# Performance work log

Hardware: AMD Instinct MI355X
Metric: run time of the kernel (lower is better)

## Reference

```python
import jax, jax.numpy as jnp
import numpy as np

B, T, H, OUT = 16384, 128, 256, 10
EPS = 1e-5


def setup_inputs() -> dict:
    key = jax.random.key(0)
    ks = jax.random.split(key, 8)
    x = jax.random.randint(ks[0], (B, T, 1), 0, 10).astype(jnp.float32)
    def lin(k, fan_out, fan_in):
        bound = 1.0 / np.sqrt(fan_in)
        kw, kb = jax.random.split(k)
        w = jax.random.uniform(kw, (fan_out, fan_in), jnp.float32, -bound, bound)
        b = jax.random.uniform(kb, (fan_out,), jnp.float32, -bound, bound)
        return w, b
    embed_w, embed_b = lin(ks[1], H, 1)
    update_w, update_b = lin(ks[2], H, H)
    out_w, out_b = lin(ks[3], OUT, H)
    return {
        "x": x,
        "embed_w": embed_w, "embed_b": embed_b,
        "update_w": update_w, "update_b": update_b,
        "gamma": jnp.ones((H,), jnp.float32), "beta": jnp.zeros((H,), jnp.float32),
        "out_w": out_w, "out_b": out_b,
    }


def _layer_norm(h, gamma, beta):
    mu = jnp.mean(h, axis=-1, keepdims=True)
    var = jnp.mean(jnp.square(h - mu), axis=-1, keepdims=True)
    return (h - mu) * jax.lax.rsqrt(var + EPS) * gamma + beta


def reference(x, embed_w, embed_b, update_w, update_b, gamma, beta, out_w, out_b):
    # embed is per-timestep independent -> precompute for all T at once: [B,T,H]
    inp_all = jnp.tanh(jnp.einsum('bti,hi->bth', x, embed_w) + embed_b)

    def step(h, inp_t):  # h:[B,H], inp_t:[B,H]
        h = jnp.tanh((inp_t + h) @ update_w.T + update_b)
        h = _layer_norm(h, gamma, beta)
        return h, None

    h0 = jnp.zeros((x.shape[0], embed_w.shape[0]), x.dtype)
    h, _ = jax.lax.scan(step, h0, jnp.swapaxes(inp_all, 0, 1))  # scan over T
    return h @ out_w.T + out_b  # [B, 10]
```

## Files before the change

kernel.cpp:

```cpp
#include <hip/hip_runtime.h>
#include <hip/hip_fp16.h>
#include <math.h>

typedef _Float16 f16;
typedef _Float16 f16x2 __attribute__((ext_vector_type(2)));
typedef _Float16 f16x8 __attribute__((ext_vector_type(8)));
typedef float f32x4 __attribute__((ext_vector_type(4)));
typedef unsigned char u8;

#define HDIM 256
#define TST 128
#define OUTD 10
#define S2LE 2.8853900817779268f

static __device__ __forceinline__ f16x2 pkrtz(float a, float b) {
  auto r = __builtin_amdgcn_cvt_pkrtz(a, b);
  return *(f16x2*)&r;
}

__global__ __launch_bounds__(256, 2) void rnn_kernel(
    const float* __restrict__ x,
    const float* __restrict__ embed_w,
    const float* __restrict__ embed_b,
    const float* __restrict__ update_w,
    const float* __restrict__ update_b,
    const float* __restrict__ gamma,
    const float* __restrict__ beta,
    const float* __restrict__ out_w,
    const float* __restrict__ out_b,
    float* __restrict__ out)
{
  __shared__ __align__(16) f16   sFR[2][8][64][8];
  __shared__ __align__(16) float sD1[10 * 260];
  __shared__ __align__(16) float sBW[HDIM];
  __shared__ __align__(16) float sRSg[HDIM];
  __shared__ float sOB[16];
  __shared__ u8    sXb[TST][32];

  const int tid = threadIdx.x;
  const int w  = tid >> 6;
  const int l  = tid & 63;
  const int q  = l >> 4;
  const int ml = l & 15;
  const int base = blockIdx.x * 32;
  const int nb = w * 64 + q * 4;
  const int m3 = ml & 3;
  const int srcl = ((ml >> 2) << 4) + ml;

  float* T0 = (float*)&sFR[0][0][0][0];

  {
    float ew = embed_w[tid], eb = embed_b[tid];
    #pragma unroll
    for (int xv = 0; xv < 10; xv++)
      T0[tid * 10 + xv] = tanhf((float)xv * ew + eb);
  }
  for (int idx = tid; idx < 32 * TST; idx += 256) {
    int col = idx >> 7, tt = idx & 127;
    sXb[tt][col] = (u8)(int)x[(size_t)(base + col) * TST + tt];
  }
  if (tid < 16) {
    float v = 0.f;
    if (tid < OUTD) {
      v = out_b[tid];
      const float* orow = out_w + tid * HDIM;
      for (int k = 0; k < HDIM; k += 4) {
        float4 wv = *(const float4*)(orow + k);
        float4 bv = *(const float4*)(beta + k);
        v = fmaf(wv.x, bv.x, fmaf(wv.y, bv.y, fmaf(wv.z, bv.z, fmaf(wv.w, bv.w, v))));
      }
    }
    sOB[tid] = v;
  }
  __syncthreads();

  {
    const int n = tid;
    const float* wrow = update_w + n * HDIM;
    float ty[10];
    #pragma unroll
    for (int xv = 0; xv < 10; xv++) ty[xv] = 0.f;
    float bw = 0.f, rsg = 0.f;
    for (int k = 0; k < HDIM; k += 4) {
      float4 wv4 = *(const float4*)(wrow + k);
      float4 b4  = *(const float4*)(beta + k);
      float4 g4  = *(const float4*)(gamma + k);
      bw  = fmaf(wv4.x, b4.x, fmaf(wv4.y, b4.y, fmaf(wv4.z, b4.z, fmaf(wv4.w, b4.w, bw))));
      rsg = fmaf(wv4.x, S2LE * g4.x, fmaf(wv4.y, S2LE * g4.y,
            fmaf(wv4.z, S2LE * g4.z, fmaf(wv4.w, S2LE * g4.w, rsg))));
      #pragma unroll
      for (int kk = 0; kk < 4; kk++) {
        float wv = ((const float*)&wv4)[kk];
        const float* t0r = T0 + (k + kk) * 10;
        #pragma unroll
        for (int xv = 0; xv < 10; xv++) ty[xv] = fmaf(wv, t0r[xv], ty[xv]);
      }
    }
    float ubn = update_b[n];
    sBW[n]  = S2LE * bw;
    sRSg[n] = rsg;
    #pragma unroll
    for (int xv = 0; xv < 10; xv++)
      sD1[xv * 260 + n] = S2LE * (ty[xv] + ubn + bw);
  }
  __syncthreads();

  f16x8 wf[4][8];
  #pragma unroll
  for (int c = 0; c < 8; c++) {
    const int k0 = c * 32 + q * 4;
    float4 g0 = *(const float4*)(gamma + k0);
    float4 g1 = *(const float4*)(gamma + k0 + 16);
    #pragma unroll
    for (int nt = 0; nt < 4; nt++) {
      const float* wrow = update_w + (w * 64 + nt * 16 + ml) * HDIM;
      float4 a0 = *(const float4*)(wrow + k0);
      float4 a1 = *(const float4*)(wrow + k0 + 16);
      f16x8 f;
      f[0]=(f16)(S2LE*g0.x*a0.x); f[1]=(f16)(S2LE*g0.y*a0.y);
      f[2]=(f16)(S2LE*g0.z*a0.z); f[3]=(f16)(S2LE*g0.w*a0.w);
      f[4]=(f16)(S2LE*g1.x*a1.x); f[5]=(f16)(S2LE*g1.y*a1.y);
      f[6]=(f16)(S2LE*g1.z*a1.z); f[7]=(f16)(S2LE*g1.w*a1.w);
      wf[nt][c] = f;
    }
  }
  f32x4 rsgr[4];
  #pragma unroll
  for (int nt = 0; nt < 4; nt++)
    rsgr[nt] = *(const f32x4*)(sRSg + nb + nt * 16);

  f16x8 ones_;
  #pragma unroll
  for (int j = 0; j < 8; j++) ones_[j] = (f16)1.f;

  f32x4 acc0[4], acc1[4];
  float s1A = 0.f, s2A = 0.f, s1B = 0.f, s2B = 0.f;

  {
    #pragma unroll
    for (int g = 0; g < 2; g++) {
      const int xv0 = (int)sXb[0][g * 16 + ml];
      const float* dp = sD1 + xv0 * 260;
      #pragma unroll
      for (int cp = 0; cp < 2; cp++) {
        union { f16x8 v8; f16x2 v2[4]; } pk;
        #pragma unroll
        for (int h = 0; h < 2; h++) {
          const int nt = 2 * cp + h;
          f32x4 dd = *(const f32x4*)(dp + nb + nt * 16);
          f32x4 bw = *(const f32x4*)(sBW + nb + nt * 16);
          float tq[4];
          #pragma unroll
          for (int r = 0; r < 4; r++) {
            float y = dd[r] - bw[r];
            float e = __builtin_amdgcn_exp2f(y);
            float tv = fmaf(-2.f, __builtin_amdgcn_rcpf(e + 1.f), 1.f);
            tq[r] = tv;
          }
          pk.v2[2 * h]     = pkrtz(tq[0], tq[1]);
          pk.v2[2 * h + 1] = pkrtz(tq[2], tq[3]);
        }
        *(f16x8*)&sFR[g][2 * w + cp][l][0] = pk.v8;
      }
    }
    __syncthreads();
  }

#define MMG3(FB, CC, CUR, NXT, ACC, AG, AS)                                    \
    { if ((CC) < 7) NXT = *(const f16x8*)((FB) + ((CC) + 1) * 512 + l * 8);    \
      ACC[0] = __builtin_amdgcn_mfma_f32_16x16x32_f16(wf[0][CC], CUR, ACC[0],0,0,0); \
      ACC[1] = __builtin_amdgcn_mfma_f32_16x16x32_f16(wf[1][CC], CUR, ACC[1],0,0,0); \
      ACC[2] = __builtin_amdgcn_mfma_f32_16x16x32_f16(wf[2][CC], CUR, ACC[2],0,0,0); \
      ACC[3] = __builtin_amdgcn_mfma_f32_16x16x32_f16(wf[3][CC], CUR, ACC[3],0,0,0); \
      AG = __builtin_amdgcn_mfma_f32_16x16x32_f16(CUR, CUR, AG, 0, 0, 0);      \
      AS = __builtin_amdgcn_mfma_f32_16x16x32_f16(ones_, CUR, AS, 0, 0, 0); }

#define SLICE(S, ACCE)                                                         \
    { _Pragma("unroll") for (int r_ = 0; r_ < 4; r_++) {                       \
        float y_ = fmaf(rs_, ACCE[S][r_], fmaf(-rm_, rsgr[S][r_], dd_[S][r_]));\
        float e_ = __builtin_amdgcn_exp2f(y_);                                 \
        tv_[S][r_] = fmaf(-2.f, __builtin_amdgcn_rcpf(e_ + 1.f), 1.f); } }

#define PACK(GE, CP)                                                           \
    { union { f16x8 v8; f16x2 v2[4]; } k_;                                     \
      k_.v2[0] = pkrtz(tv_[2*(CP)][0],   tv_[2*(CP)][1]);                      \
      k_.v2[1] = pkrtz(tv_[2*(CP)][2],   tv_[2*(CP)][3]);                      \
      k_.v2[2] = pkrtz(tv_[2*(CP)+1][0], tv_[2*(CP)+1][1]);                    \
      k_.v2[3] = pkrtz(tv_[2*(CP)+1][2], tv_[2*(CP)+1][3]);                    \
      *(f16x8*)&sFR[GE][2 * w + (CP)][l][0] = k_.v8; }

#define PHASE(TE, GM, GE, XOFF, ACCM, ACCE, S1E, S2E, S1O, S2O)                \
  {                                                                            \
    const int xv_ = (int)sXb[TE][XOFF + ml];                                   \
    const float* dp_ = sD1 + xv_ * 260 + nb;                                   \
    f32x4 dd_[4];                                                              \
    _Pragma("unroll") for (int n_ = 0; n_ < 4; n_++)                           \
      dd_[n_] = *(const f32x4*)(dp_ + n_ * 16);                                \
    const f16* fbm_ = &sFR[GM][0][0][0];                                       \
    f16x8 rA_ = *(const f16x8*)(fbm_ + l * 8);                                 \
    f16x8 rB_;                                                                 \
    f32x4 aG_ = {0.f,0.f,0.f,0.f}, aS_ = {0.f,0.f,0.f,0.f};                    \
    _Pragma("unroll") for (int n_ = 0; n_ < 4; n_++)                           \
      ACCM[n_] = (f32x4){0.f, 0.f, 0.f, 0.f};                                  \
    f32x4 tv_[4];                                                              \
    __builtin_amdgcn_s_setprio(1);                                             \
    MMG3(fbm_, 0, rA_, rB_, ACCM, aG_, aS_)                                    \
    MMG3(fbm_, 1, rB_, rA_, ACCM, aG_, aS_)                                    \
    float mu_ = (S1E) * (1.f / 256.f);                                         \
    float rs_ = __frsqrt_rn(fmaf((S2E), 1.f / 256.f, -mu_ * mu_) + 1e-5f);     \
    float rm_ = rs_ * mu_;                                                     \
    SLICE(0, ACCE)                                                             \
    MMG3(fbm_, 2, rA_, rB_, ACCM, aG_, aS_)                                    \
    MMG3(fbm_, 3, rB_, rA_, ACCM, aG_, aS_)                                    \
    SLICE(1, ACCE)                                                             \
    PACK(GE, 0)                                                                \
    MMG3(fbm_, 4, rA_, rB_, ACCM, aG_, aS_)                                    \
    MMG3(fbm_, 5, rB_, rA_, ACCM, aG_, aS_)                                    \
    SLICE(2, ACCE)                                                             \
    MMG3(fbm_, 6, rA_, rB_, ACCM, aG_, aS_)                                    \
    MMG3(fbm_, 7, rB_, rA_, ACCM, aG_, aS_)                                    \
    SLICE(3, ACCE)                                                             \
    PACK(GE, 1)                                                                \
    __builtin_amdgcn_s_setprio(0);                                             \
    __syncthreads();                                                           \
    S1O = aS_[0];                                                              \
    float sel_ = aG_[0];                                                       \
    sel_ = (m3 == 1) ? aG_[1] : sel_;                                          \
    sel_ = (m3 == 2) ? aG_[2] : sel_;                                          \
    sel_ = (m3 == 3) ? aG_[3] : sel_;                                          \
    S2O = __shfl(sel_, srcl, 64);                                              \
  }

  {
    const f16* fbm_ = &sFR[0][0][0][0];
    f16x8 rA_ = *(const f16x8*)(fbm_ + l * 8);
    f16x8 rB_;
    f32x4 aG_ = {0.f,0.f,0.f,0.f}, aS_ = {0.f,0.f,0.f,0.f};
    #pragma unroll
    for (int n_ = 0; n_ < 4; n_++) acc0[n_] = (f32x4){0.f, 0.f, 0.f, 0.f};
    MMG3(fbm_, 0, rA_, rB_, acc0, aG_, aS_)
    MMG3(fbm_, 1, rB_, rA_, acc0, aG_, aS_)
    MMG3(fbm_, 2, rA_, rB_, acc0, aG_, aS_)
    MMG3(fbm_, 3, rB_, rA_, acc0, aG_, aS_)
    MMG3(fbm_, 4, rA_, rB_, acc0, aG_, aS_)
    MMG3(fbm_, 5, rB_, rA_, acc0, aG_, aS_)
    MMG3(fbm_, 6, rA_, rB_, acc0, aG_, aS_)
    MMG3(fbm_, 7, rB_, rA_, acc0, aG_, aS_)
    __syncthreads();
    s1A = aS_[0];
    float sel_ = aG_[0];
    sel_ = (m3 == 1) ? aG_[1] : sel_;
    sel_ = (m3 == 2) ? aG_[2] : sel_;
    sel_ = (m3 == 3) ? aG_[3] : sel_;
    s2A = __shfl(sel_, srcl, 64);
  }

  #pragma unroll 1
  for (int t = 1; t <= 127; t++) {
    PHASE(t, 1, 0, 0,  acc1, acc0, s1A, s2A, s1B, s2B)
    PHASE(t, 0, 1, 16, acc0, acc1, s1B, s2B, s1A, s2A)
  }

  {
    f32x4 aG2 = {0.f,0.f,0.f,0.f}, aS2 = {0.f,0.f,0.f,0.f};
    const f16* fb1 = &sFR[1][0][0][0];
    #pragma unroll
    for (int c = 0; c < 8; c++) {
      f16x8 rr = *(const f16x8*)(fb1 + c * 512 + l * 8);
      aG2 = __builtin_amdgcn_mfma_f32_16x16x32_f16(rr, rr, aG2, 0, 0, 0);
      aS2 = __builtin_amdgcn_mfma_f32_16x16x32_f16(ones_, rr, aS2, 0, 0, 0);
    }
    float s1C = aS2[0];
    float sel2 = aG2[0];
    sel2 = (m3 == 1) ? aG2[1] : sel2;
    sel2 = (m3 == 2) ? aG2[2] : sel2;
    sel2 = (m3 == 3) ? aG2[3] : sel2;
    float s2C = __shfl(sel2, srcl, 64);

    float rsF[2], nmF[2];
    {
      float mu = s1A * (1.f / 256.f);
      float ve = fmaf(s2A, 1.f / 256.f, -mu * mu) + 1e-5f;
      rsF[0] = __frsqrt_rn(ve); nmF[0] = -rsF[0] * mu;
      float mu1 = s1C * (1.f / 256.f);
      float ve1 = fmaf(s2C, 1.f / 256.f, -mu1 * mu1) + 1e-5f;
      rsF[1] = __frsqrt_rn(ve1); nmF[1] = -rsF[1] * mu1;
    }
    f16x8 fin[2][2];
    #pragma unroll
    for (int g = 0; g < 2; g++)
      #pragma unroll
      for (int cp = 0; cp < 2; cp++)
        fin[g][cp] = *(const f16x8*)&sFR[g][2 * w + cp][l][0];

    f16* sOW = (f16*)sD1;
    for (int idx = tid; idx < 512; idx += 256) {
      int c = idx >> 6, l2 = idx & 63, q2 = l2 >> 4, o = l2 & 15;
      int k0 = c * 32 + q2 * 4;
      f16x8 f;
      #pragma unroll
      for (int j = 0; j < 8; j++) f[j] = (f16)0.f;
      if (o < OUTD) {
        const float* orow = out_w + o * HDIM;
        float4 a0 = *(const float4*)(orow + k0);
        float4 a1 = *(const float4*)(orow + k0 + 16);
        float4 g0 = *(const float4*)(gamma + k0);
        float4 g1 = *(const float4*)(gamma + k0 + 16);
        f[0]=(f16)(g0.x*a0.x); f[1]=(f16)(g0.y*a0.y); f[2]=(f16)(g0.z*a0.z); f[3]=(f16)(g0.w*a0.w);
        f[4]=(f16)(g1.x*a1.x); f[5]=(f16)(g1.y*a1.y); f[6]=(f16)(g1.z*a1.z); f[7]=(f16)(g1.w*a1.w);
      }
      *(f16x8*)(sOW + idx * 8) = f;
    }
    __syncthreads();

    float* sOut = (float*)&sFR[0][0][0][0];
    #pragma unroll
    for (int g = 0; g < 2; g++) {
      f32x4 aO = {0.f, 0.f, 0.f, 0.f};
      #pragma unroll
      for (int cp = 0; cp < 2; cp++) {
        f16x8 af;
        #pragma unroll
        for (int j = 0; j < 8; j++)
          af[j] = (f16)fmaf(rsF[g], (float)fin[g][cp][j], nmF[g]);
        f16x8 of = *(const f16x8*)(sOW + ((size_t)(2 * w + cp) * 64 + l) * 8);
        aO = __builtin_amdgcn_mfma_f32_16x16x32_f16(of, af, aO, 0, 0, 0);
      }
      #pragma unroll
      for (int r = 0; r < 4; r++)
        sOut[((g * 4 + w) * 16 + ml) * 16 + q * 4 + r] = aO[r];
    }
    __syncthreads();
    for (int idx = tid; idx < 32 * OUTD; idx += 256) {
      int m = idx / OUTD, o = idx - m * OUTD;
      int g = m >> 4, mm = m & 15;
      float s = 0.f;
      #pragma unroll
      for (int ww = 0; ww < 4; ww++) s += sOut[((g * 4 + ww) * 16 + mm) * 16 + o];
      out[(size_t)(base + m) * OUTD + o] = s + sOB[o];
    }
  }
}

extern "C" void kernel_launch(void* const* d_in, const int* in_sizes, int n_in,
                              void* d_out, int out_size, void* d_ws, size_t ws_size,
                              hipStream_t stream) {
  const float* x   = (const float*)d_in[0];
  const float* ew  = (const float*)d_in[1];
  const float* eb  = (const float*)d_in[2];
  const float* uw  = (const float*)d_in[3];
  const float* ub  = (const float*)d_in[4];
  const float* g   = (const float*)d_in[5];
  const float* be  = (const float*)d_in[6];
  const float* ow  = (const float*)d_in[7];
  const float* ob  = (const float*)d_in[8];
  float* out = (float*)d_out;

  const int B = in_sizes[0] / TST;
  const int grid = B / 32;
  hipLaunchKernelGGL(rnn_kernel, dim3(grid), dim3(256), 0, stream,
                     x, ew, eb, uw, ub, g, be, ow, ob, out);
}
```

Before: 353.9 us.

## Split hidden dimension across eight waves with LDS-reduced layernorm statistics

Doubles the block to 512 threads (8 waves), so each wave owns 32 hidden units instead of 64. This halves the per-wave update-weight fragments held in registers and the MFMA work on each step's critical path. Because each wave now sees only a slice of the hidden state, the layernorm sum and sum-of-squares are computed per slice with MFMAs, written to a shared-memory table, and summed by every thread on the next phase. The intent is more waves per CU to hide latency and shorter per-step chains, at the cost of extra LDS traffic, more threads joining each per-step barrier, and a higher register-pressure target from launch_bounds(512,4).

```diff
diff --git a/kernel.cpp b/kernel.cpp
--- a/kernel.cpp
+++ b/kernel.cpp
@@ -18,7 +18,7 @@
   return *(f16x2*)&r;
 }
 
-__global__ __launch_bounds__(256, 2) void rnn_kernel(
+__global__ __launch_bounds__(512, 4) void rnn_kernel(
     const float* __restrict__ x,
     const float* __restrict__ embed_w,
     const float* __restrict__ embed_b,
@@ -34,6 +34,7 @@
   __shared__ __align__(16) float sD1[10 * 260];
   __shared__ __align__(16) float sBW[HDIM];
   __shared__ __align__(16) float sRSg[HDIM];
+  __shared__ __align__(16) float sST[2][16][10][2];
   __shared__ float sOB[16];
   __shared__ u8    sXb[TST][32];
 
@@ -42,20 +43,20 @@
   const int l  = tid & 63;
   const int q  = l >> 4;
   const int ml = l & 15;
+  const int m3 = ml & 3;
   const int base = blockIdx.x * 32;
-  const int nb = w * 64 + q * 4;
-  const int m3 = ml & 3;
-  const int srcl = ((ml >> 2) << 4) + ml;
+  const int nb = w * 32 + q * 4;
+  const int diagw = (q == (ml >> 2));
 
   float* T0 = (float*)&sFR[0][0][0][0];
 
-  {
+  if (tid < 256) {
     float ew = embed_w[tid], eb = embed_b[tid];
     #pragma unroll
     for (int xv = 0; xv < 10; xv++)
       T0[tid * 10 + xv] = tanhf((float)xv * ew + eb);
   }
-  for (int idx = tid; idx < 32 * TST; idx += 256) {
+  for (int idx = tid; idx < 32 * TST; idx += 512) {
     int col = idx >> 7, tt = idx & 127;
     sXb[tt][col] = (u8)(int)x[(size_t)(base + col) * TST + tt];
   }
@@ -74,7 +75,7 @@
   }
   __syncthreads();
 
-  {
+  if (tid < 256) {
     const int n = tid;
     const float* wrow = update_w + n * HDIM;
     float ty[10];
@@ -105,15 +106,15 @@
   }
   __syncthreads();
 
-  f16x8 wf[4][8];
+  f16x8 wf[2][8];
   #pragma unroll
   for (int c = 0; c < 8; c++) {
     const int k0 = c * 32 + q * 4;
     float4 g0 = *(const float4*)(gamma + k0);
     float4 g1 = *(const float4*)(gamma + k0 + 16);
     #pragma unroll
-    for (int nt = 0; nt < 4; nt++) {
-      const float* wrow = update_w + (w * 64 + nt * 16 + ml) * HDIM;
+    for (int nt = 0; nt < 2; nt++) {
+      const float* wrow = update_w + (w * 32 + nt * 16 + ml) * HDIM;
       float4 a0 = *(const float4*)(wrow + k0);
       float4 a1 = *(const float4*)(wrow + k0 + 16);
       f16x8 f;
@@ -124,178 +125,171 @@
       wf[nt][c] = f;
     }
   }
-  f32x4 rsgr[4];
-  #pragma unroll
-  for (int nt = 0; nt < 4; nt++)
-    rsgr[nt] = *(const f32x4*)(sRSg + nb + nt * 16);
-
-  f16x8 ones_;
-  #pragma unroll
-  for (int j = 0; j < 8; j++) ones_[j] = (f16)1.f;
-
-  f32x4 acc0[4], acc1[4];
-  float s1A = 0.f, s2A = 0.f, s1B = 0.f, s2B = 0.f;
+  f32x4 rsgr[2];
+  rsgr[0] = *(const f32x4*)(sRSg + nb);
+  rsgr[1] = *(const f32x4*)(sRSg + nb + 16);
+
+  f32x4 acc0[2], acc1[2];
 
   {
     #pragma unroll
     for (int g = 0; g < 2; g++) {
       const int xv0 = (int)sXb[0][g * 16 + ml];
       const float* dp = sD1 + xv0 * 260;
-      #pragma unroll
-      for (int cp = 0; cp < 2; cp++) {
-        union { f16x8 v8; f16x2 v2[4]; } pk;
-        #pragma unroll
-        for (int h = 0; h < 2; h++) {
-          const int nt = 2 * cp + h;
-          f32x4 dd = *(const f32x4*)(dp + nb + nt * 16);
-          f32x4 bw = *(const f32x4*)(sBW + nb + nt * 16);
-          float tq[4];
-          #pragma unroll
-          for (int r = 0; r < 4; r++) {
-            float y = dd[r] - bw[r];
-            float e = __builtin_amdgcn_exp2f(y);
-            float tv = fmaf(-2.f, __builtin_amdgcn_rcpf(e + 1.f), 1.f);
-            tq[r] = tv;
-          }
-          pk.v2[2 * h]     = pkrtz(tq[0], tq[1]);
-          pk.v2[2 * h + 1] = pkrtz(tq[2], tq[3]);
-        }
-        *(f16x8*)&sFR[g][2 * w + cp][l][0] = pk.v8;
+      f32x4 bw0 = *(const f32x4*)(sBW + nb);
+      f32x4 bw1 = *(const f32x4*)(sBW + nb + 16);
+      f32x4 dd0 = *(const f32x4*)(dp + nb);
+      f32x4 dd1 = *(const f32x4*)(dp + nb + 16);
+      float t0v[4], t1v[4];
+      #pragma unroll
+      for (int r = 0; r < 4; r++) {
+        float y0 = dd0[r] - bw0[r];
+        float e0 = __builtin_amdgcn_exp2f(y0);
+        t0v[r] = fmaf(-2.f, __builtin_amdgcn_rcpf(e0 + 1.f), 1.f);
+        float y1 = dd1[r] - bw1[r];
+        float e1 = __builtin_amdgcn_exp2f(y1);
+        t1v[r] = fmaf(-2.f, __builtin_amdgcn_rcpf(e1 + 1.f), 1.f);
       }
-    }
-    __syncthreads();
-  }
-
-#define MMG3(FB, CC, CUR, NXT, ACC, AG, AS)                                    \
+      union { f16x8 v8; f16x2 v2[4]; } pk;
+      pk.v2[0] = pkrtz(t0v[0], t0v[1]);
+      pk.v2[1] = pkrtz(t0v[2], t0v[3]);
+      pk.v2[2] = pkrtz(t1v[0], t1v[1]);
+      pk.v2[3] = pkrtz(t1v[2], t1v[3]);
+      *(f16x8*)&sFR[g][w][l][0] = pk.v8;
+    }
+    __syncthreads();
+  }
+
+#define MMG2(FB, CC, CUR, NXT, ACC)                                            \
     { if ((CC) < 7) NXT = *(const f16x8*)((FB) + ((CC) + 1) * 512 + l * 8);    \
       ACC[0] = __builtin_amdgcn_mfma_f32_16x16x32_f16(wf[0][CC], CUR, ACC[0],0,0,0); \
-      ACC[1] = __builtin_amdgcn_mfma_f32_16x16x32_f16(wf[1][CC], CUR, ACC[1],0,0,0); \
-      ACC[2] = __builtin_amdgcn_mfma_f32_16x16x32_f16(wf[2][CC], CUR, ACC[2],0,0,0); \
-      ACC[3] = __builtin_amdgcn_mfma_f32_16x16x32_f16(wf[3][CC], CUR, ACC[3],0,0,0); \
-      AG = __builtin_amdgcn_mfma_f32_16x16x32_f16(CUR, CUR, AG, 0, 0, 0);      \
-      AS = __builtin_amdgcn_mfma_f32_16x16x32_f16(ones_, CUR, AS, 0, 0, 0); }
-
-#define SLICE(S, ACCE)                                                         \
+      ACC[1] = __builtin_amdgcn_mfma_f32_16x16x32_f16(wf[1][CC], CUR, ACC[1],0,0,0); }
+
+#define STATMM(RO, AG, AS)                                                     \
+    { f16x8 ones_;                                                             \
+      _Pragma("unroll") for (int j_ = 0; j_ < 8; j_++) ones_[j_] = (f16)1.f;   \
+      AG = __builtin_amdgcn_mfma_f32_16x16x32_f16(RO, RO, AG, 0, 0, 0);        \
+      AS = __builtin_amdgcn_mfma_f32_16x16x32_f16(ones_, RO, AS, 0, 0, 0); }
+
+#define STATWR(G, AG, AS)                                                      \
+    { float sel_ = AG[0];                                                      \
+      sel_ = (m3 == 1) ? AG[1] : sel_;                                         \
+      sel_ = (m3 == 2) ? AG[2] : sel_;                                         \
+      sel_ = (m3 == 3) ? AG[3] : sel_;                                         \
+      if (diagw) *(float2*)&sST[G][ml][w][0] = make_float2(AS[0], sel_); }
+
+#define STATRD(G, S1, S2)                                                      \
+    { const float* sp_ = &sST[G][ml][0][0];                                    \
+      f32x4 a0_ = *(const f32x4*)(sp_);                                        \
+      f32x4 a1_ = *(const f32x4*)(sp_ + 4);                                    \
+      f32x4 a2_ = *(const f32x4*)(sp_ + 8);                                    \
+      f32x4 a3_ = *(const f32x4*)(sp_ + 12);                                   \
+      S1 = ((a0_[0] + a0_[2]) + (a1_[0] + a1_[2]))                             \
+         + ((a2_[0] + a2_[2]) + (a3_[0] + a3_[2]));                            \
+      S2 = ((a0_[1] + a0_[3]) + (a1_[1] + a1_[3]))                             \
+         + ((a2_[1] + a2_[3]) + (a3_[1] + a3_[3])); }
+
+#define SLICEH(H, ACCE, DD, TVV)                                               \
     { _Pragma("unroll") for (int r_ = 0; r_ < 4; r_++) {                       \
-        float y_ = fmaf(rs_, ACCE[S][r_], fmaf(-rm_, rsgr[S][r_], dd_[S][r_]));\
+        float y_ = fmaf(rs_, ACCE[H][r_], fmaf(-rm_, rsgr[H][r_], DD[r_]));    \
         float e_ = __builtin_amdgcn_exp2f(y_);                                 \
-        tv_[S][r_] = fmaf(-2.f, __builtin_amdgcn_rcpf(e_ + 1.f), 1.f); } }
-
-#define PACK(GE, CP)                                                           \
-    { union { f16x8 v8; f16x2 v2[4]; } k_;                                     \
-      k_.v2[0] = pkrtz(tv_[2*(CP)][0],   tv_[2*(CP)][1]);                      \
-      k_.v2[1] = pkrtz(tv_[2*(CP)][2],   tv_[2*(CP)][3]);                      \
-      k_.v2[2] = pkrtz(tv_[2*(CP)+1][0], tv_[2*(CP)+1][1]);                    \
-      k_.v2[3] = pkrtz(tv_[2*(CP)+1][2], tv_[2*(CP)+1][3]);                    \
-      *(f16x8*)&sFR[GE][2 * w + (CP)][l][0] = k_.v8; }
-
-#define PHASE(TE, GM, GE, XOFF, ACCM, ACCE, S1E, S2E, S1O, S2O)                \
+        TVV[r_] = fmaf(-2.f, __builtin_amdgcn_rcpf(e_ + 1.f), 1.f); } }
+
+#define PHASE(TE, GM, GE, XOFF, ACCM, ACCE)                                    \
   {                                                                            \
+    float s1_, s2_;                                                            \
+    STATRD(GE, s1_, s2_)                                                       \
     const int xv_ = (int)sXb[TE][XOFF + ml];                                   \
     const float* dp_ = sD1 + xv_ * 260 + nb;                                   \
-    f32x4 dd_[4];                                                              \
-    _Pragma("unroll") for (int n_ = 0; n_ < 4; n_++)                           \
-      dd_[n_] = *(const f32x4*)(dp_ + n_ * 16);                                \
+    f32x4 dd0_ = *(const f32x4*)(dp_);                                         \
+    f32x4 dd1_ = *(const f32x4*)(dp_ + 16);                                    \
     const f16* fbm_ = &sFR[GM][0][0][0];                                       \
+    f16x8 rOwn_ = *(const f16x8*)(fbm_ + w * 512 + l * 8);                     \
+    f32x4 aG_ = {0.f,0.f,0.f,0.f}, aS_ = {0.f,0.f,0.f,0.f};                    \
+    STATMM(rOwn_, aG_, aS_)                                                    \
     f16x8 rA_ = *(const f16x8*)(fbm_ + l * 8);                                 \
     f16x8 rB_;                                                                 \
-    f32x4 aG_ = {0.f,0.f,0.f,0.f}, aS_ = {0.f,0.f,0.f,0.f};                    \
-    _Pragma("unroll") for (int n_ = 0; n_ < 4; n_++)                           \
-      ACCM[n_] = (f32x4){0.f, 0.f, 0.f, 0.f};                                  \
-    f32x4 tv_[4];                                                              \
+    ACCM[0] = (f32x4){0.f, 0.f, 0.f, 0.f};                                     \
+    ACCM[1] = (f32x4){0.f, 0.f, 0.f, 0.f};                                     \
     __builtin_amdgcn_s_setprio(1);                                             \
-    MMG3(fbm_, 0, rA_, rB_, ACCM, aG_, aS_)                                    \
-    MMG3(fbm_, 1, rB_, rA_, ACCM, aG_, aS_)                                    \
-    float mu_ = (S1E) * (1.f / 256.f);                                         \
-    float rs_ = __frsqrt_rn(fmaf((S2E), 1.f / 256.f, -mu_ * mu_) + 1e-5f);     \
+    MMG2(fbm_, 0, rA_, rB_, ACCM)                                              \
+    MMG2(fbm_, 1, rB_, rA_, ACCM)                                              \
+    float mu_ = s1_ * (1.f / 256.f);                                           \
+    float rs_ = __frsqrt_rn(fmaf(s2_, 1.f / 256.f, -mu_ * mu_) + 1e-5f);       \
     float rm_ = rs_ * mu_;                                                     \
-    SLICE(0, ACCE)                                                             \
-    MMG3(fbm_, 2, rA_, rB_, ACCM, aG_, aS_)                                    \
-    MMG3(fbm_, 3, rB_, rA_, ACCM, aG_, aS_)                                    \
-    SLICE(1, ACCE)                                                             \
-    PACK(GE, 0)                                                                \
-    MMG3(fbm_, 4, rA_, rB_, ACCM, aG_, aS_)                                    \
-    MMG3(fbm_, 5, rB_, rA_, ACCM, aG_, aS_)                                    \
-    SLICE(2, ACCE)                                                             \
-    MMG3(fbm_, 6, rA_, rB_, ACCM, aG_, aS_)                                    \
-    MMG3(fbm_, 7, rB_, rA_, ACCM, aG_, aS_)                                    \
-    SLICE(3, ACCE)                                                             \
-    PACK(GE, 1)                                                                \
+    float t0_[4], t1_[4];                                                      \
+    MMG2(fbm_, 2, rA_, rB_, ACCM)                                              \
+    SLICEH(0, ACCE, dd0_, t0_)                                                 \
+    MMG2(fbm_, 3, rB_, rA_, ACCM)                                              \
+    MMG2(fbm_, 4, rA_, rB_, ACCM)                                              \
+    SLICEH(1, ACCE, dd1_, t1_)                                                 \
+    MMG2(fbm_, 5, rB_, rA_, ACCM)                                              \
+    {                                                                          \
+      union { f16x8 v8; f16x2 v2[4]; } k_;                                     \
+      k_.v2[0] = pkrtz(t0_[0], t0_[1]);                                        \
+      k_.v2[1] = pkrtz(t0_[2], t0_[3]);                                        \
+      k_.v2[2] = pkrtz(t1_[0], t1_[1]);                                        \
+      k_.v2[3] = pkrtz(t1_[2], t1_[3]);                                        \
+      *(f16x8*)&sFR[GE][w][l][0] = k_.v8;                                      \
+    }                                                                          \
+    MMG2(fbm_, 6, rA_, rB_, ACCM)                                              \
+    MMG2(fbm_, 7, rB_, rA_, ACCM)                                              \
     __builtin_amdgcn_s_setprio(0);                                             \
+    STATWR(GM, aG_, aS_)                                                       \
     __syncthreads();                                                           \
-    S1O = aS_[0];                                                              \
-    float sel_ = aG_[0];                                                       \
-    sel_ = (m3 == 1) ? aG_[1] : sel_;                                          \
-    sel_ = (m3 == 2) ? aG_[2] : sel_;                                          \
-    sel_ = (m3 == 3) ? aG_[3] : sel_;                                          \
-    S2O = __shfl(sel_, srcl, 64);                                              \
   }
 
   {
     const f16* fbm_ = &sFR[0][0][0][0];
+    f16x8 rOwn_ = *(const f16x8*)(fbm_ + w * 512 + l * 8);
+    f32x4 aG_ = {0.f,0.f,0.f,0.f}, aS_ = {0.f,0.f,0.f,0.f};
+    STATMM(rOwn_, aG_, aS_)
     f16x8 rA_ = *(const f16x8*)(fbm_ + l * 8);
     f16x8 rB_;
-    f32x4 aG_ = {0.f,0.f,0.f,0.f}, aS_ = {0.f,0.f,0.f,0.f};
-    #pragma unroll
-    for (int n_ = 0; n_ < 4; n_++) acc0[n_] = (f32x4){0.f, 0.f, 0.f, 0.f};
-    MMG3(fbm_, 0, rA_, rB_, acc0, aG_, aS_)
-    MMG3(fbm_, 1, rB_, rA_, acc0, aG_, aS_)
-    MMG3(fbm_, 2, rA_, rB_, acc0, aG_, aS_)
-    MMG3(fbm_, 3, rB_, rA_, acc0, aG_, aS_)
-    MMG3(fbm_, 4, rA_, rB_, acc0, aG_, aS_)
-    MMG3(fbm_, 5, rB_, rA_, acc0, aG_, aS_)
-    MMG3(fbm_, 6, rA_, rB_, acc0, aG_, aS_)
-    MMG3(fbm_, 7, rB_, rA_, acc0, aG_, aS_)
-    __syncthreads();
-    s1A = aS_[0];
-    float sel_ = aG_[0];
-    sel_ = (m3 == 1) ? aG_[1] : sel_;
-    sel_ = (m3 == 2) ? aG_[2] : sel_;
-    sel_ = (m3 == 3) ? aG_[3] : sel_;
-    s2A = __shfl(sel_, srcl, 64);
+    acc0[0] = (f32x4){0.f, 0.f, 0.f, 0.f};
+    acc0[1] = (f32x4){0.f, 0.f, 0.f, 0.f};
+    MMG2(fbm_, 0, rA_, rB_, acc0)
+    MMG2(fbm_, 1, rB_, rA_, acc0)
+    MMG2(fbm_, 2, rA_, rB_, acc0)
+    MMG2(fbm_, 3, rB_, rA_, acc0)
+    MMG2(fbm_, 4, rA_, rB_, acc0)
+    MMG2(fbm_, 5, rB_, rA_, acc0)
+    MMG2(fbm_, 6, rA_, rB_, acc0)
+    MMG2(fbm_, 7, rB_, rA_, acc0)
+    STATWR(0, aG_, aS_)
+    __syncthreads();
   }
 
   #pragma unroll 1
   for (int t = 1; t <= 127; t++) {
-    PHASE(t, 1, 0, 0,  acc1, acc0, s1A, s2A, s1B, s2B)
-    PHASE(t, 0, 1, 16, acc0, acc1, s1B, s2B, s1A, s2A)
+    PHASE(t, 1, 0, 0,  acc1, acc0)
+    PHASE(t, 0, 1, 16, acc0, acc1)
   }
 
   {
+    f16x8 fin1 = *(const f16x8*)&sFR[1][w][l][0];
     f32x4 aG2 = {0.f,0.f,0.f,0.f}, aS2 = {0.f,0.f,0.f,0.f};
-    const f16* fb1 = &sFR[1][0][0][0];
-    #pragma unroll
-    for (int c = 0; c < 8; c++) {
-      f16x8 rr = *(const f16x8*)(fb1 + c * 512 + l * 8);
-      aG2 = __builtin_amdgcn_mfma_f32_16x16x32_f16(rr, rr, aG2, 0, 0, 0);
-      aS2 = __builtin_amdgcn_mfma_f32_16x16x32_f16(ones_, rr, aS2, 0, 0, 0);
-    }
-    float s1C = aS2[0];
-    float sel2 = aG2[0];
-    sel2 = (m3 == 1) ? aG2[1] : sel2;
-    sel2 = (m3 == 2) ? aG2[2] : sel2;
-    sel2 = (m3 == 3) ? aG2[3] : sel2;
-    float s2C = __shfl(sel2, srcl, 64);
+    STATMM(fin1, aG2, aS2)
+    STATWR(1, aG2, aS2)
+    f16x8 fin0 = *(const f16x8*)&sFR[0][w][l][0];
+    __syncthreads();
 
     float rsF[2], nmF[2];
     {
-      float mu = s1A * (1.f / 256.f);
-      float ve = fmaf(s2A, 1.f / 256.f, -mu * mu) + 1e-5f;
+      float s1, s2;
+      STATRD(0, s1, s2)
+      float mu = s1 * (1.f / 256.f);
+      float ve = fmaf(s2, 1.f / 256.f, -mu * mu) + 1e-5f;
       rsF[0] = __frsqrt_rn(ve); nmF[0] = -rsF[0] * mu;
-      float mu1 = s1C * (1.f / 256.f);
-      float ve1 = fmaf(s2C, 1.f / 256.f, -mu1 * mu1) + 1e-5f;
-      rsF[1] = __frsqrt_rn(ve1); nmF[1] = -rsF[1] * mu1;
-    }
-    f16x8 fin[2][2];
-    #pragma unroll
-    for (int g = 0; g < 2; g++)
-      #pragma unroll
-      for (int cp = 0; cp < 2; cp++)
-        fin[g][cp] = *(const f16x8*)&sFR[g][2 * w + cp][l][0];
+      STATRD(1, s1, s2)
+      mu = s1 * (1.f / 256.f);
+      ve = fmaf(s2, 1.f / 256.f, -mu * mu) + 1e-5f;
+      rsF[1] = __frsqrt_rn(ve); nmF[1] = -rsF[1] * mu;
+    }
 
     f16* sOW = (f16*)sD1;
-    for (int idx = tid; idx < 512; idx += 256) {
-      int c = idx >> 6, l2 = idx & 63, q2 = l2 >> 4, o = l2 & 15;
+    {
+      int c = tid >> 6, l2 = tid & 63, q2 = l2 >> 4, o = l2 & 15;
       int k0 = c * 32 + q2 * 4;
       f16x8 f;
       #pragma unroll
@@ -309,34 +303,33 @@
         f[0]=(f16)(g0.x*a0.x); f[1]=(f16)(g0.y*a0.y); f[2]=(f16)(g0.z*a0.z); f[3]=(f16)(g0.w*a0.w);
         f[4]=(f16)(g1.x*a1.x); f[5]=(f16)(g1.y*a1.y); f[6]=(f16)(g1.z*a1.z); f[7]=(f16)(g1.w*a1.w);
       }
-      *(f16x8*)(sOW + idx * 8) = f;
+      *(f16x8*)(sOW + (size_t)tid * 8) = f;
     }
     __syncthreads();
 
     float* sOut = (float*)&sFR[0][0][0][0];
+    f16x8 of = *(const f16x8*)(sOW + ((size_t)w * 64 + l) * 8);
     #pragma unroll
     for (int g = 0; g < 2; g++) {
+      f16x8 fin = (g == 0) ? fin0 : fin1;
+      f16x8 af;
+      #pragma unroll
+      for (int j = 0; j < 8; j++)
+        af[j] = (f16)fmaf(rsF[g], (float)fin[j], nmF[g]);
       f32x4 aO = {0.f, 0.f, 0.f, 0.f};
-      #pragma unroll
-      for (int cp = 0; cp < 2; cp++) {
-        f16x8 af;
-        #pragma unroll
-        for (int j = 0; j < 8; j++)
-          af[j] = (f16)fmaf(rsF[g], (float)fin[g][cp][j], nmF[g]);
-        f16x8 of = *(const f16x8*)(sOW + ((size_t)(2 * w + cp) * 64 + l) * 8);
-        aO = __builtin_amdgcn_mfma_f32_16x16x32_f16(of, af, aO, 0, 0, 0);
-      }
+      aO = __builtin_amdgcn_mfma_f32_16x16x32_f16(of, af, aO, 0, 0, 0);
       #pragma unroll
       for (int r = 0; r < 4; r++)
-        sOut[((g * 4 + w) * 16 + ml) * 16 + q * 4 + r] = aO[r];
-    }
-    __syncthreads();
-    for (int idx = tid; idx < 32 * OUTD; idx += 256) {
-      int m = idx / OUTD, o = idx - m * OUTD;
+        sOut[(((g * 8 + w) * 16) + ml) * 16 + q * 4 + r] = aO[r];
+    }
+    __syncthreads();
+    if (tid < 32 * OUTD) {
+      int m = tid / OUTD, o = tid - m * OUTD;
       int g = m >> 4, mm = m & 15;
       float s = 0.f;
       #pragma unroll
-      for (int ww = 0; ww < 4; ww++) s += sOut[((g * 4 + ww) * 16 + mm) * 16 + o];
+      for (int ww = 0; ww < 8; ww++)
+        s += sOut[(((g * 8 + ww) * 16) + mm) * 16 + o];
       out[(size_t)(base + m) * OUTD + o] = s + sOB[o];
     }
   }
@@ -358,6 +351,6 @@
 
   const int B = in_sizes[0] / TST;
   const int grid = B / 32;
-  hipLaunchKernelGGL(rnn_kernel, dim3(grid), dim3(256), 0, stream,
+  hipLaunchKernelGGL(rnn_kernel, dim3(grid), dim3(512), 0, stream,
                      x, ew, eb, uw, ub, g, be, ow, ob, out);
 }
```

Measured after the change: 356.2 us. About the same (+0.7%).

## Compute LayerNorm stats per-wave on owned chunks and reduce via shared memory

Applied to the files above, without the earlier changes.

Each wave used to compute sum and sum-of-squares MFMAs over all 8 K-chunks of the hidden state, which is redundant work across the 4 waves. Now each wave computes stats only over its own 2 chunks after packing, writes partials to a small shared buffer, and the next phase reads and sums the 4 partials. This removes 12 of the 16 stat MFMAs each wave issues per phase. In exchange it adds extra LDS reads and writes plus a dependency on the existing barrier to publish the partial stats.

```diff
diff --git a/kernel.cpp b/kernel.cpp
--- a/kernel.cpp
+++ b/kernel.cpp
@@ -34,6 +34,7 @@
   __shared__ __align__(16) float sD1[10 * 260];
   __shared__ __align__(16) float sBW[HDIM];
   __shared__ __align__(16) float sRSg[HDIM];
+  __shared__ __align__(16) float sST[2][16][10][2];
   __shared__ float sOB[16];
   __shared__ u8    sXb[TST][32];
 
@@ -42,10 +43,10 @@
   const int l  = tid & 63;
   const int q  = l >> 4;
   const int ml = l & 15;
+  const int m3 = ml & 3;
   const int base = blockIdx.x * 32;
   const int nb = w * 64 + q * 4;
-  const int m3 = ml & 3;
-  const int srcl = ((ml >> 2) << 4) + ml;
+  const int diagw = (q == (ml >> 2));
 
   float* T0 = (float*)&sFR[0][0][0][0];
 
@@ -132,9 +133,9 @@
   f16x8 ones_;
   #pragma unroll
   for (int j = 0; j < 8; j++) ones_[j] = (f16)1.f;
+  const f32x4 zeros_ = {0.f, 0.f, 0.f, 0.f};
 
   f32x4 acc0[4], acc1[4];
-  float s1A = 0.f, s2A = 0.f, s1B = 0.f, s2B = 0.f;
 
   {
     #pragma unroll
@@ -166,14 +167,44 @@
     __syncthreads();
   }
 
-#define MMG3(FB, CC, CUR, NXT, ACC, AG, AS)                                    \
+#define MMG(FB, CC, CUR, NXT, ACC)                                             \
     { if ((CC) < 7) NXT = *(const f16x8*)((FB) + ((CC) + 1) * 512 + l * 8);    \
       ACC[0] = __builtin_amdgcn_mfma_f32_16x16x32_f16(wf[0][CC], CUR, ACC[0],0,0,0); \
       ACC[1] = __builtin_amdgcn_mfma_f32_16x16x32_f16(wf[1][CC], CUR, ACC[1],0,0,0); \
       ACC[2] = __builtin_amdgcn_mfma_f32_16x16x32_f16(wf[2][CC], CUR, ACC[2],0,0,0); \
-      ACC[3] = __builtin_amdgcn_mfma_f32_16x16x32_f16(wf[3][CC], CUR, ACC[3],0,0,0); \
-      AG = __builtin_amdgcn_mfma_f32_16x16x32_f16(CUR, CUR, AG, 0, 0, 0);      \
-      AS = __builtin_amdgcn_mfma_f32_16x16x32_f16(ones_, CUR, AS, 0, 0, 0); }
+      ACC[3] = __builtin_amdgcn_mfma_f32_16x16x32_f16(wf[3][CC], CUR, ACC[3],0,0,0); }
+
+#define GSEL(AG, SEL)                                                          \
+    { SEL = AG[0];                                                             \
+      SEL = (m3 == 1) ? AG[1] : SEL;                                           \
+      SEL = (m3 == 2) ? AG[2] : SEL;                                           \
+      SEL = (m3 == 3) ? AG[3] : SEL; }
+
+#define STATRD(G, S1, S2)                                                      \
+    { const float* sp_ = &sST[G][ml][0][0];                                    \
+      f32x4 a0_ = *(const f32x4*)(sp_);                                        \
+      f32x4 a1_ = *(const f32x4*)(sp_ + 4);                                    \
+      f32x4 a2_ = *(const f32x4*)(sp_ + 8);                                    \
+      f32x4 a3_ = *(const f32x4*)(sp_ + 12);                                   \
+      S1 = ((a0_[0] + a0_[2]) + (a1_[0] + a1_[2]))                             \
+         + ((a2_[0] + a2_[2]) + (a3_[0] + a3_[2]));                            \
+      S2 = ((a0_[1] + a0_[3]) + (a1_[1] + a1_[3]))                             \
+         + ((a2_[1] + a2_[3]) + (a3_[1] + a3_[3])); }
+
+#define STATOWN(FB, G)                                                         \
+    { f16x8 ro0_ = *(const f16x8*)((FB) + (2 * w) * 512 + l * 8);              \
+      f16x8 ro1_ = *(const f16x8*)((FB) + (2 * w + 1) * 512 + l * 8);          \
+      f32x4 aG0_ = __builtin_amdgcn_mfma_f32_16x16x32_f16(ro0_, ro0_, zeros_,0,0,0); \
+      f32x4 aS0_ = __builtin_amdgcn_mfma_f32_16x16x32_f16(ones_, ro0_, zeros_,0,0,0); \
+      f32x4 aG1_ = __builtin_amdgcn_mfma_f32_16x16x32_f16(ro1_, ro1_, zeros_,0,0,0); \
+      f32x4 aS1_ = __builtin_amdgcn_mfma_f32_16x16x32_f16(ones_, ro1_, zeros_,0,0,0); \
+      float sel0_, sel1_;                                                      \
+      GSEL(aG0_, sel0_)                                                        \
+      GSEL(aG1_, sel1_)                                                        \
+      if (diagw)                                                               \
+        *(f32x4*)&sST[G][ml][2 * w][0] =                                       \
+            (f32x4){aS0_[0], sel0_, aS1_[0], sel1_};                           \
+    }
 
 #define SLICE(S, ACCE)                                                         \
     { _Pragma("unroll") for (int r_ = 0; r_ < 4; r_++) {                       \
@@ -189,8 +220,10 @@
       k_.v2[3] = pkrtz(tv_[2*(CP)+1][2], tv_[2*(CP)+1][3]);                    \
       *(f16x8*)&sFR[GE][2 * w + (CP)][l][0] = k_.v8; }
 
-#define PHASE(TE, GM, GE, XOFF, ACCM, ACCE, S1E, S2E, S1O, S2O)                \
+#define PHASE(TE, GM, GE, XOFF, ACCM, ACCE)                                    \
   {                                                                            \
+    float s1_, s2_;                                                            \
+    STATRD(GE, s1_, s2_)                                                       \
     const int xv_ = (int)sXb[TE][XOFF + ml];                                   \
     const float* dp_ = sD1 + xv_ * 260 + nb;                                   \
     f32x4 dd_[4];                                                              \
@@ -199,99 +232,83 @@
     const f16* fbm_ = &sFR[GM][0][0][0];                                       \
     f16x8 rA_ = *(const f16x8*)(fbm_ + l * 8);                                 \
     f16x8 rB_;                                                                 \
-    f32x4 aG_ = {0.f,0.f,0.f,0.f}, aS_ = {0.f,0.f,0.f,0.f};                    \
-    _Pragma("unroll") for (int n_ = 0; n_ < 4; n_++)                           \
-      ACCM[n_] = (f32x4){0.f, 0.f, 0.f, 0.f};                                  \
     f32x4 tv_[4];                                                              \
     __builtin_amdgcn_s_setprio(1);                                             \
-    MMG3(fbm_, 0, rA_, rB_, ACCM, aG_, aS_)                                    \
-    MMG3(fbm_, 1, rB_, rA_, ACCM, aG_, aS_)                                    \
-    float mu_ = (S1E) * (1.f / 256.f);                                         \
-    float rs_ = __frsqrt_rn(fmaf((S2E), 1.f / 256.f, -mu_ * mu_) + 1e-5f);     \
+    rB_ = *(const f16x8*)(fbm_ + 512 + l * 8);                                 \
+    ACCM[0] = __builtin_amdgcn_mfma_f32_16x16x32_f16(wf[0][0], rA_, zeros_,0,0,0); \
+    ACCM[1] = __builtin_amdgcn_mfma_f32_16x16x32_f16(wf[1][0], rA_, zeros_,0,0,0); \
+    ACCM[2] = __builtin_amdgcn_mfma_f32_16x16x32_f16(wf[2][0], rA_, zeros_,0,0,0); \
+    ACCM[3] = __builtin_amdgcn_mfma_f32_16x16x32_f16(wf[3][0], rA_, zeros_,0,0,0); \
+    MMG(fbm_, 1, rB_, rA_, ACCM)                                               \
+    float mu_ = s1_ * (1.f / 256.f);                                           \
+    float rs_ = __frsqrt_rn(fmaf(s2_, 1.f / 256.f, -mu_ * mu_) + 1e-5f);       \
     float rm_ = rs_ * mu_;                                                     \
     SLICE(0, ACCE)                                                             \
-    MMG3(fbm_, 2, rA_, rB_, ACCM, aG_, aS_)                                    \
-    MMG3(fbm_, 3, rB_, rA_, ACCM, aG_, aS_)                                    \
+    MMG(fbm_, 2, rA_, rB_, ACCM)                                               \
+    MMG(fbm_, 3, rB_, rA_, ACCM)                                               \
     SLICE(1, ACCE)                                                             \
     PACK(GE, 0)                                                                \
-    MMG3(fbm_, 4, rA_, rB_, ACCM, aG_, aS_)                                    \
-    MMG3(fbm_, 5, rB_, rA_, ACCM, aG_, aS_)                                    \
+    MMG(fbm_, 4, rA_, rB_, ACCM)                                               \
+    MMG(fbm_, 5, rB_, rA_, ACCM)                                               \
     SLICE(2, ACCE)                                                             \
-    MMG3(fbm_, 6, rA_, rB_, ACCM, aG_, aS_)                                    \
-    MMG3(fbm_, 7, rB_, rA_, ACCM, aG_, aS_)                                    \
+    MMG(fbm_, 6, rA_, rB_, ACCM)                                               \
+    MMG(fbm_, 7, rB_, rA_, ACCM)                                               \
     SLICE(3, ACCE)                                                             \
     PACK(GE, 1)                                                                \
+    STATOWN(fbm_, GM)                                                          \
     __builtin_amdgcn_s_setprio(0);                                             \
     __syncthreads();                                                           \
-    S1O = aS_[0];                                                              \
-    float sel_ = aG_[0];                                                       \
-    sel_ = (m3 == 1) ? aG_[1] : sel_;                                          \
-    sel_ = (m3 == 2) ? aG_[2] : sel_;                                          \
-    sel_ = (m3 == 3) ? aG_[3] : sel_;                                          \
-    S2O = __shfl(sel_, srcl, 64);                                              \
   }
 
   {
     const f16* fbm_ = &sFR[0][0][0][0];
     f16x8 rA_ = *(const f16x8*)(fbm_ + l * 8);
     f16x8 rB_;
-    f32x4 aG_ = {0.f,0.f,0.f,0.f}, aS_ = {0.f,0.f,0.f,0.f};
-    #pragma unroll
-    for (int n_ = 0; n_ < 4; n_++) acc0[n_] = (f32x4){0.f, 0.f, 0.f, 0.f};
-    MMG3(fbm_, 0, rA_, rB_, acc0, aG_, aS_)
-    MMG3(fbm_, 1, rB_, rA_, acc0, aG_, aS_)
-    MMG3(fbm_, 2, rA_, rB_, acc0, aG_, aS_)
-    MMG3(fbm_, 3, rB_, rA_, acc0, aG_, aS_)
-    MMG3(fbm_, 4, rA_, rB_, acc0, aG_, aS_)
-    MMG3(fbm_, 5, rB_, rA_, acc0, aG_, aS_)
-    MMG3(fbm_, 6, rA_, rB_, acc0, aG_, aS_)
-    MMG3(fbm_, 7, rB_, rA_, acc0, aG_, aS_)
-    __syncthreads();
-    s1A = aS_[0];
-    float sel_ = aG_[0];
-    sel_ = (m3 == 1) ? aG_[1] : sel_;
-    sel_ = (m3 == 2) ? aG_[2] : sel_;
-    sel_ = (m3 == 3) ? aG_[3] : sel_;
-    s2A = __shfl(sel_, srcl, 64);
+    rB_ = *(const f16x8*)(fbm_ + 512 + l * 8);
+    acc0[0] = __builtin_amdgcn_mfma_f32_16x16x32_f16(wf[0][0], rA_, zeros_,0,0,0);
+    acc0[1] = __builtin_amdgcn_mfma_f32_16x16x32_f16(wf[1][0], rA_, zeros_,0,0,0);
+    acc0[2] = __builtin_amdgcn_mfma_f32_16x16x32_f16(wf[2][0], rA_, zeros_,0,0,0);
+    acc0[3] = __builtin_amdgcn_mfma_f32_16x16x32_f16(wf[3][0], rA_, zeros_,0,0,0);
+    MMG(fbm_, 1, rB_, rA_, acc0)
+    MMG(fbm_, 2, rA_, rB_, acc0)
+    MMG(fbm_, 3, rB_, rA_, acc0)
+    MMG(fbm_, 4, rA_, rB_, acc0)
+    MMG(fbm_, 5, rB_, rA_, acc0)
+    MMG(fbm_, 6, rA_, rB_, acc0)
+    MMG(fbm_, 7, rB_, rA_, acc0)
+    STATOWN(fbm_, 0)
+    __syncthreads();
   }
 
   #pragma unroll 1
   for (int t = 1; t <= 127; t++) {
-    PHASE(t, 1, 0, 0,  acc1, acc0, s1A, s2A, s1B, s2B)
-    PHASE(t, 0, 1, 16, acc0, acc1, s1B, s2B, s1A, s2A)
-  }
-
-  {
-    f32x4 aG2 = {0.f,0.f,0.f,0.f}, aS2 = {0.f,0.f,0.f,0.f};
+    PHASE(t, 1, 0, 0,  acc1, acc0)
+    PHASE(t, 0, 1, 16, acc0, acc1)
+  }
+
+  {
     const f16* fb1 = &sFR[1][0][0][0];
-    #pragma unroll
-    for (int c = 0; c < 8; c++) {
-      f16x8 rr = *(const f16x8*)(fb1 + c * 512 + l * 8);
-      aG2 = __builtin_amdgcn_mfma_f32_16x16x32_f16(rr, rr, aG2, 0, 0, 0);
-      aS2 = __builtin_amdgcn_mfma_f32_16x16x32_f16(ones_, rr, aS2, 0, 0, 0);
-    }
-    float s1C = aS2[0];
-    float sel2 = aG2[0];
-    sel2 = (m3 == 1) ? aG2[1] : sel2;
-    sel2 = (m3 == 2) ? aG2[2] : sel2;
-    sel2 = (m3 == 3) ? aG2[3] : sel2;
-    float s2C = __shfl(sel2, srcl, 64);
+    STATOWN(fb1, 1)
+    f16x8 fin0[2], fin1[2];
+    #pragma unroll
+    for (int cp = 0; cp < 2; cp++) {
+      fin0[cp] = *(const f16x8*)&sFR[0][2 * w + cp][l][0];
+      fin1[cp] = *(const f16x8*)&sFR[1][2 * w + cp][l][0];
+    }
+    __syncthreads();
 
     float rsF[2], nmF[2];
     {
-      float mu = s1A * (1.f / 256.f);
-      float ve = fmaf(s2A, 1.f / 256.f, -mu * mu) + 1e-5f;
+      float s1, s2;
+      STATRD(0, s1, s2)
+      float mu = s1 * (1.f / 256.f);
+      float ve = fmaf(s2, 1.f / 256.f, -mu * mu) + 1e-5f;
       rsF[0] = __frsqrt_rn(ve); nmF[0] = -rsF[0] * mu;
-      float mu1 = s1C * (1.f / 256.f);
-      float ve1 = fmaf(s2C, 1.f / 256.f, -mu1 * mu1) + 1e-5f;
-      rsF[1] = __frsqrt_rn(ve1); nmF[1] = -rsF[1] * mu1;
-    }
-    f16x8 fin[2][2];
-    #pragma unroll
-    for (int g = 0; g < 2; g++)
-      #pragma unroll
-      for (int cp = 0; cp < 2; cp++)
-        fin[g][cp] = *(const f16x8*)&sFR[g][2 * w + cp][l][0];
+      STATRD(1, s1, s2)
+      mu = s1 * (1.f / 256.f);
+      ve = fmaf(s2, 1.f / 256.f, -mu * mu) + 1e-5f;
+      rsF[1] = __frsqrt_rn(ve); nmF[1] = -rsF[1] * mu;
+    }
 
     f16* sOW = (f16*)sD1;
     for (int idx = tid; idx < 512; idx += 256) {
@@ -316,13 +333,14 @@
     float* sOut = (float*)&sFR[0][0][0][0];
     #pragma unroll
     for (int g = 0; g < 2; g++) {
-      f32x4 aO = {0.f, 0.f, 0.f, 0.f};
+      f32x4 aO = zeros_;
       #pragma unroll
       for (int cp = 0; cp < 2; cp++) {
+        f16x8 fr = (g == 0) ? fin0[cp] : fin1[cp];
         f16x8 af;
         #pragma unroll
         for (int j = 0; j < 8; j++)
-          af[j] = (f16)fmaf(rsF[g], (float)fin[g][cp][j], nmF[g]);
+          af[j] = (f16)fmaf(rsF[g], (float)fr[j], nmF[g]);
         f16x8 of = *(const f16x8*)(sOW + ((size_t)(2 * w + cp) * 64 + l) * 8);
         aO = __builtin_amdgcn_mfma_f32_16x16x32_f16(of, af, aO, 0, 0, 0);
       }
```

Measured after the change: 317.9 us, median of 2. 10.2% less time.
